# Performance work log

Hardware: AMD Instinct MI355X
Metric: run time of the kernel (lower is better)

The kernel has to match this reference:

```python
import jax, jax.numpy as jnp
import numpy as np

N_NODES = 100000
N_EDGES = 1600000
IN_DIM = 32
OUT_DIM = 64


def setup_inputs() -> dict:
    key = jax.random.key(0)
    k1, k2, k3, k4, k5 = jax.random.split(key, 5)
    feature = jax.random.normal(k1, (N_NODES, IN_DIM), dtype=jnp.float32)
    src = jax.random.randint(k2, (N_EDGES,), 0, N_NODES, dtype=jnp.int32)
    dst = jax.random.randint(k3, (N_EDGES,), 0, N_NODES, dtype=jnp.int32)
    W = jax.random.normal(k4, (IN_DIM, OUT_DIM), dtype=jnp.float32) * (1.0 / np.sqrt(IN_DIM))
    b = jax.random.normal(k5, (OUT_DIM,), dtype=jnp.float32) * 0.01
    return {"feature": feature, "src": src, "dst": dst, "W": W, "b": b}


def reference(feature, src, dst, W, b):
    # copy_u + sum: gather source features along edges, segment-sum into dst nodes
    msgs = feature[src]  # [E, in_dim]
    h_neigh = jax.ops.segment_sum(msgs, dst, num_segments=N_NODES)  # [N, in_dim]
    # linear projection
    return h_neigh @ W + b  # [N, out_dim]
```

## Files before the change

kernel.cpp:

```cpp
#include <hip/hip_runtime.h>

#define IN_DIM 32
#define OUT_DIM 64

__global__ __launch_bounds__(256) void mpnn_scatter_kernel(
    const float* __restrict__ feature,
    const int* __restrict__ src,
    const int* __restrict__ dst,
    float* __restrict__ h,
    int n_edges) {
    long long tid = (long long)blockIdx.x * blockDim.x + threadIdx.x;
    long long total = (long long)n_edges * IN_DIM;
    if (tid >= total) return;
    int e = (int)(tid >> 5);
    int d = (int)(tid & 31);
    int s = src[e];
    int t = dst[e];
    float v = feature[(long long)s * IN_DIM + d];
    atomicAdd(&h[(long long)t * IN_DIM + d], v);
}

__global__ __launch_bounds__(256) void mpnn_proj_kernel(
    const float* __restrict__ h,
    const float* __restrict__ W,
    const float* __restrict__ b,
    float* __restrict__ out,
    int n_nodes) {
    __shared__ float Ws[IN_DIM * OUT_DIM];
    __shared__ float hs[4][IN_DIM];
    int tx = threadIdx.x;

    for (int i = tx; i < IN_DIM * OUT_DIM; i += 256) Ws[i] = W[i];

    int row0 = blockIdx.x * 4;
    if (tx < 4 * IN_DIM) {
        int r = tx >> 5, k = tx & 31;
        int row = row0 + r;
        hs[r][k] = (row < n_nodes) ? h[(long long)row * IN_DIM + k] : 0.0f;
    }
    __syncthreads();

    int col = tx & 63;
    int r = tx >> 6;
    int row = row0 + r;
    if (row >= n_nodes) return;

    float acc = b[col];
#pragma unroll
    for (int k = 0; k < IN_DIM; ++k)
        acc += hs[r][k] * Ws[k * OUT_DIM + col];

    out[(long long)row * OUT_DIM + col] = acc;
}

extern "C" void kernel_launch(void* const* d_in, const int* in_sizes, int n_in,
                              void* d_out, int out_size, void* d_ws, size_t ws_size,
                              hipStream_t stream) {
    const float* feature = (const float*)d_in[0];
    const int* src = (const int*)d_in[1];
    const int* dst = (const int*)d_in[2];
    const float* W = (const float*)d_in[3];
    const float* b = (const float*)d_in[4];
    float* out = (float*)d_out;

    int n_nodes = in_sizes[0] / IN_DIM;
    int n_edges = in_sizes[1];

    float* h = (float*)d_ws;

    hipMemsetAsync(h, 0, (size_t)n_nodes * IN_DIM * sizeof(float), stream);

    long long total = (long long)n_edges * IN_DIM;
    int threads = 256;
    int blocks = (int)((total + threads - 1) / threads);
    mpnn_scatter_kernel<<<blocks, threads, 0, stream>>>(feature, src, dst, h, n_edges);

    int pblocks = (n_nodes + 3) / 4;
    mpnn_proj_kernel<<<pblocks, 256, 0, stream>>>(h, W, b, out, n_nodes);
}
```

Measured before the change: 276.0 us.

## Build CSR by destination each call and fuse gather-sum with projection

Replaces the per-element float atomic scatter with a CSR build on every call: a histogram of dst, a two-level prefix scan, and an atomic-cursor scatter of src indices. A fused kernel then gathers and sums neighbor features per node in registers and applies the linear projection directly, which removes the intermediate h buffer and its 32 float atomics per edge. The trade-off is five extra small kernel launches and integer atomics for the histogram and scatter. Summation order within a node is now nondeterministic, as it was before.

```diff
diff --git a/kernel.cpp b/kernel.cpp
--- a/kernel.cpp
+++ b/kernel.cpp
@@ -2,55 +2,114 @@
 
 #define IN_DIM 32
 #define OUT_DIM 64
+#define NB_SCAN 391
 
-__global__ __launch_bounds__(256) void mpnn_scatter_kernel(
-    const float* __restrict__ feature,
-    const int* __restrict__ src,
-    const int* __restrict__ dst,
-    float* __restrict__ h,
-    int n_edges) {
-    long long tid = (long long)blockIdx.x * blockDim.x + threadIdx.x;
-    long long total = (long long)n_edges * IN_DIM;
-    if (tid >= total) return;
-    int e = (int)(tid >> 5);
-    int d = (int)(tid & 31);
-    int s = src[e];
-    int t = dst[e];
-    float v = feature[(long long)s * IN_DIM + d];
-    atomicAdd(&h[(long long)t * IN_DIM + d], v);
+__global__ __launch_bounds__(256) void hist_kernel(
+    const int* __restrict__ dst, int* __restrict__ counts, int n_edges) {
+    int e = blockIdx.x * 256 + threadIdx.x;
+    if (e < n_edges) atomicAdd(&counts[dst[e]], 1);
 }
 
-__global__ __launch_bounds__(256) void mpnn_proj_kernel(
-    const float* __restrict__ h,
-    const float* __restrict__ W,
-    const float* __restrict__ b,
-    float* __restrict__ out,
-    int n_nodes) {
+__global__ __launch_bounds__(256) void scan1_kernel(
+    const int* __restrict__ counts, int* __restrict__ row_start,
+    int* __restrict__ block_sums, int n) {
+    __shared__ int tmp[256];
+    int tx = threadIdx.x;
+    int idx = blockIdx.x * 256 + tx;
+    int v = (idx < n) ? counts[idx] : 0;
+    tmp[tx] = v;
+    __syncthreads();
+    for (int off = 1; off < 256; off <<= 1) {
+        int t = (tx >= off) ? tmp[tx - off] : 0;
+        __syncthreads();
+        tmp[tx] += t;
+        __syncthreads();
+    }
+    if (idx < n) row_start[idx] = tmp[tx] - v;
+    if (tx == 255) block_sums[blockIdx.x] = tmp[255];
+}
+
+__global__ __launch_bounds__(512) void scan2_kernel(int* __restrict__ block_sums, int nb) {
+    __shared__ int tmp[512];
+    int tx = threadIdx.x;
+    int v = (tx < nb) ? block_sums[tx] : 0;
+    tmp[tx] = v;
+    __syncthreads();
+    for (int off = 1; off < 512; off <<= 1) {
+        int t = (tx >= off) ? tmp[tx - off] : 0;
+        __syncthreads();
+        tmp[tx] += t;
+        __syncthreads();
+    }
+    if (tx < nb) block_sums[tx] = tmp[tx] - v;
+}
+
+__global__ __launch_bounds__(256) void finalize_kernel(
+    int* __restrict__ row_start, const int* __restrict__ block_sums,
+    int* __restrict__ cursor, int n, int n_edges) {
+    int idx = blockIdx.x * 256 + threadIdx.x;
+    if (idx < n) {
+        int v = row_start[idx] + block_sums[blockIdx.x];
+        row_start[idx] = v;
+        cursor[idx] = v;
+    }
+    if (blockIdx.x == 0 && threadIdx.x == 0) row_start[n] = n_edges;
+}
+
+__global__ __launch_bounds__(256) void scatter_kernel(
+    const int* __restrict__ src, const int* __restrict__ dst,
+    int* __restrict__ cursor, int* __restrict__ edge_src, int n_edges) {
+    int e = blockIdx.x * 256 + threadIdx.x;
+    if (e < n_edges) {
+        int pos = atomicAdd(&cursor[dst[e]], 1);
+        edge_src[pos] = src[e];
+    }
+}
+
+__global__ __launch_bounds__(256) void gather_proj_kernel(
+    const float* __restrict__ feature, const int* __restrict__ row_start,
+    const int* __restrict__ edge_src, const float* __restrict__ W,
+    const float* __restrict__ b, float* __restrict__ out, int n_nodes) {
     __shared__ float Ws[IN_DIM * OUT_DIM];
-    __shared__ float hs[4][IN_DIM];
+    __shared__ float bs[OUT_DIM];
+    __shared__ float hs[8][IN_DIM];
     int tx = threadIdx.x;
 
     for (int i = tx; i < IN_DIM * OUT_DIM; i += 256) Ws[i] = W[i];
+    if (tx < OUT_DIM) bs[tx] = b[tx];
 
-    int row0 = blockIdx.x * 4;
-    if (tx < 4 * IN_DIM) {
-        int r = tx >> 5, k = tx & 31;
-        int row = row0 + r;
-        hs[r][k] = (row < n_nodes) ? h[(long long)row * IN_DIM + k] : 0.0f;
+    int slot = tx >> 5, lane = tx & 31;
+    int node = blockIdx.x * 8 + slot;
+    float acc = 0.0f;
+    if (node < n_nodes) {
+        int s0 = row_start[node], s1 = row_start[node + 1];
+        int i = s0;
+        for (; i + 4 <= s1; i += 4) {
+            int ea = edge_src[i], eb = edge_src[i + 1];
+            int ec = edge_src[i + 2], ed = edge_src[i + 3];
+            float fa = feature[(long long)ea * IN_DIM + lane];
+            float fb = feature[(long long)eb * IN_DIM + lane];
+            float fc = feature[(long long)ec * IN_DIM + lane];
+            float fd = feature[(long long)ed * IN_DIM + lane];
+            acc += fa + fb + fc + fd;
+        }
+        for (; i < s1; ++i) acc += feature[(long long)edge_src[i] * IN_DIM + lane];
     }
+    hs[slot][lane] = acc;
     __syncthreads();
 
-    int col = tx & 63;
-    int r = tx >> 6;
-    int row = row0 + r;
-    if (row >= n_nodes) return;
-
-    float acc = b[col];
+    int node0 = blockIdx.x * 8;
 #pragma unroll
-    for (int k = 0; k < IN_DIM; ++k)
-        acc += hs[r][k] * Ws[k * OUT_DIM + col];
-
-    out[(long long)row * OUT_DIM + col] = acc;
+    for (int it = 0; it < 2; ++it) {
+        int idx = tx + it * 256;
+        int sl = idx >> 6, col = idx & 63;
+        int n2 = node0 + sl;
+        if (n2 >= n_nodes) continue;
+        float a = bs[col];
+#pragma unroll
+        for (int k = 0; k < IN_DIM; ++k) a += hs[sl][k] * Ws[k * OUT_DIM + col];
+        out[(long long)n2 * OUT_DIM + col] = a;
+    }
 }
 
 extern "C" void kernel_launch(void* const* d_in, const int* in_sizes, int n_in,
@@ -66,15 +125,22 @@
     int n_nodes = in_sizes[0] / IN_DIM;
     int n_edges = in_sizes[1];
 
-    float* h = (float*)d_ws;
+    int* counts = (int*)d_ws;
+    int* row_start = counts + n_nodes;
+    int* cursor = row_start + n_nodes + 1;
+    int* block_sums = cursor + n_nodes;
+    int* edge_src = block_sums + 512;
 
-    hipMemsetAsync(h, 0, (size_t)n_nodes * IN_DIM * sizeof(float), stream);
+    (void)hipMemsetAsync(counts, 0, (size_t)n_nodes * sizeof(int), stream);
 
-    long long total = (long long)n_edges * IN_DIM;
-    int threads = 256;
-    int blocks = (int)((total + threads - 1) / threads);
-    mpnn_scatter_kernel<<<blocks, threads, 0, stream>>>(feature, src, dst, h, n_edges);
+    int eb = (n_edges + 255) / 256;
+    int nb = (n_nodes + 255) / 256;
+    hist_kernel<<<eb, 256, 0, stream>>>(dst, counts, n_edges);
+    scan1_kernel<<<nb, 256, 0, stream>>>(counts, row_start, block_sums, n_nodes);
+    scan2_kernel<<<1, 512, 0, stream>>>(block_sums, nb);
+    finalize_kernel<<<nb, 256, 0, stream>>>(row_start, block_sums, cursor, n_nodes, n_edges);
+    scatter_kernel<<<eb, 256, 0, stream>>>(src, dst, cursor, edge_src, n_edges);
 
-    int pblocks = (n_nodes + 3) / 4;
-    mpnn_proj_kernel<<<pblocks, 256, 0, stream>>>(h, W, b, out, n_nodes);
+    int gblocks = (n_nodes + 7) / 8;
+    gather_proj_kernel<<<gblocks, 256, 0, stream>>>(feature, row_start, edge_src, W, b, out, n_nodes);
 }
```

New measurement: 324.6 us. 17.6% more time.
